# Kernel tuning notes

Measured on AMD Instinct MI355X. Metric: run time of the kernel, lower is better.

The kernel has to match this reference:

```python
import jax, jax.numpy as jnp
import numpy as np

N_U = 50000; N_I = 50000; F = 128; H = 128; E = 800000; G = 512; C = 16; L = 3
EPS = 1e-5


def setup_inputs() -> dict:
    key = jax.random.key(0)
    ks = jax.random.split(key, 22)
    s = 1.0 / np.sqrt(H)
    inp = {}
    inp["x_user"] = jax.random.normal(ks[0], (N_U, F), jnp.float32)
    inp["x_item"] = jax.random.normal(ks[1], (N_I, F), jnp.float32)
    inp["edge_u2i"] = jnp.stack([jax.random.randint(ks[2], (E,), 0, N_U),
                                 jax.random.randint(ks[3], (E,), 0, N_I)])
    inp["edge_i2u"] = jnp.stack([jax.random.randint(ks[4], (E,), 0, N_I),
                                 jax.random.randint(ks[5], (E,), 0, N_U)])
    inp["batch_user"] = jnp.sort(jax.random.randint(ks[6], (N_U,), 0, G))
    inp["batch_item"] = jnp.sort(jax.random.randint(ks[7], (N_I,), 0, G))
    # GraphConv params per layer per relation (in-dim == hidden == 128, so stackable)
    inp["Wrel_u2i"] = jax.random.uniform(ks[8], (L, H, F), jnp.float32, -s, s)
    inp["Wroot_u2i"] = jax.random.uniform(ks[9], (L, H, F), jnp.float32, -s, s)
    inp["b_u2i"] = jax.random.uniform(ks[10], (L, H), jnp.float32, -s, s)
    inp["Wrel_i2u"] = jax.random.uniform(ks[11], (L, H, F), jnp.float32, -s, s)
    inp["Wroot_i2u"] = jax.random.uniform(ks[12], (L, H, F), jnp.float32, -s, s)
    inp["b_i2u"] = jax.random.uniform(ks[13], (L, H), jnp.float32, -s, s)
    # BatchNorm (one module per node type, reused across layers)
    inp["bn_g_user"] = jnp.ones((H,), jnp.float32)
    inp["bn_b_user"] = jnp.zeros((H,), jnp.float32)
    inp["bn_g_item"] = jnp.ones((H,), jnp.float32)
    inp["bn_b_item"] = jnp.zeros((H,), jnp.float32)
    # per-layer classifier heads
    inp["fc_W"] = jax.random.uniform(ks[14], (L, C, H), jnp.float32, -s, s)
    inp["fc_b"] = jax.random.uniform(ks[15], (L, C), jnp.float32, -s, s)
    return inp


def _graph_conv(x_src, x_dst, edge, Wrel, Wroot, b, n_dst):
    # GraphConv, aggr='add': W_rel @ sum_{j in N(i)} x_j + W_root @ x_i + b
    agg = jax.ops.segment_sum(x_src[edge[0]], edge[1], num_segments=n_dst)  # [n_dst, F]
    return agg @ Wrel.T + x_dst @ Wroot.T + b


def _bn(x, g, b):
    # BatchNorm1d over nodes, training-mode batch statistics (biased var)
    m = x.mean(0)
    v = jnp.mean((x - m) ** 2, axis=0)
    return (x - m) * jax.lax.rsqrt(v + EPS) * g + b


def reference(x_user, x_item, edge_u2i, edge_i2u, batch_user, batch_item,
              Wrel_u2i, Wroot_u2i, b_u2i, Wrel_i2u, Wroot_i2u, b_i2u,
              bn_g_user, bn_b_user, bn_g_item, bn_b_item, fc_W, fc_b):
    batch_all = jnp.concatenate([batch_user, batch_item])
    cnt = jax.ops.segment_sum(jnp.ones((N_U + N_I,), jnp.float32), batch_all,
                              num_segments=G)
    cnt = jnp.maximum(cnt, 1.0)[:, None]
    feats = []
    xu, xi = x_user, x_item
    for l in range(L):
        new_i = _graph_conv(xu, xi, edge_u2i, Wrel_u2i[l], Wroot_u2i[l], b_u2i[l], N_I)
        new_u = _graph_conv(xi, xu, edge_i2u, Wrel_i2u[l], Wroot_i2u[l], b_i2u[l], N_U)
        xu = _bn(jax.nn.relu(new_u), bn_g_user, bn_b_user)
        xi = _bn(jax.nn.relu(new_i), bn_g_item, bn_b_item)
        pooled = jax.ops.segment_sum(jnp.concatenate([xu, xi], 0), batch_all,
                                     num_segments=G) / cnt  # global mean pool [G, H]
        feats.append(pooled)
    feats = jnp.stack(feats)  # [L, G, H]
    # eval mode: F.dropout is identity; per-layer linear heads
    logits = jnp.einsum('lgh,lch->lgc', feats, fc_W) + fc_b[:, None, :]  # [L, G, C]
    return (logits, feats)
```

## Files before the change

kernel.cpp:

```cpp
#include <hip/hip_runtime.h>

#define NN 50000
#define FD 128
#define NE 800000
#define NG 512
#define NC 16
#define NL 3
#define NTOT 100000
#define NBLK 391
#define NBUCK 196
#define CAP 10240
#define BINTILE 2048
#define NBINBLK 782
#define BNEPS 1e-5f
#define LOGITS_N (NL*NG*NC)

typedef unsigned short u16;
typedef unsigned char u8;
typedef __attribute__((ext_vector_type(8))) short short8;
typedef __attribute__((ext_vector_type(4))) float f32x4;

#define OFF_GCNT     0ul
#define OFF_BCUR     4096ul
#define OFF_ACC      5120ul
#define MEMSET_BYTES 7168ul
#define OFF_USTART   7680ul
#define OFF_ISTART   10240ul
#define OFF_INVCNT   12800ul
#define OFF_BNSC     14848ul
#define OFF_BNSH     15872ul
#define OFF_ROWRANGE 16896ul
#define OFF_WB       817152ul
#define OFF_CSR      1210368ul
#define OFF_N0I      9238528ul
#define OFF_N0U      22038528ul
#define OFF_N1U      34838528ul
#define OFF_N1I      47638528ul
#define OFF_XU0      60438528ul
#define OFF_XI0      73238528ul
#define OFF_WBS      73238528ul
#define OFF_BVEC     73369600ul

static __device__ __forceinline__ float bf2f(u16 v) {
  return __uint_as_float(((unsigned)v) << 16);
}
static __device__ __forceinline__ u16 f2bf(float f) {
  unsigned u = __float_as_uint(f);
  return (u16)((u + 0x7FFFu + ((u >> 16) & 1u)) >> 16);
}
template<int RELU>
static __device__ __forceinline__ void accT8(float* a, int4 v) {
  unsigned w[4] = {(unsigned)v.x, (unsigned)v.y, (unsigned)v.z, (unsigned)v.w};
  #pragma unroll
  for (int i = 0; i < 4; i++) {
    float lo = __uint_as_float(w[i] << 16);
    float hi = __uint_as_float(w[i] & 0xffff0000u);
    if (RELU) { lo = lo > 0.f ? lo : 0.f; hi = hi > 0.f ? hi : 0.f; }
    a[2*i]   += lo;
    a[2*i+1] += hi;
  }
}
static __device__ __forceinline__ void unp8(float* a, int4 v) {
  a[0] = __uint_as_float(((unsigned)v.x) << 16);
  a[1] = __uint_as_float(((unsigned)v.x) & 0xffff0000u);
  a[2] = __uint_as_float(((unsigned)v.y) << 16);
  a[3] = __uint_as_float(((unsigned)v.y) & 0xffff0000u);
  a[4] = __uint_as_float(((unsigned)v.z) << 16);
  a[5] = __uint_as_float(((unsigned)v.z) & 0xffff0000u);
  a[6] = __uint_as_float(((unsigned)v.w) << 16);
  a[7] = __uint_as_float(((unsigned)v.w) & 0xffff0000u);
}
static __device__ __forceinline__ int relu2(int w) {
  int lo = (w & 0x00008000) ? 0 : (w & 0x0000FFFF);
  int hi = (w < 0)          ? 0 : (int)(w & 0xFFFF0000u);
  return lo | hi;
}

__global__ __launch_bounds__(256) void k_hist_batch(const int* __restrict__ bu,
                                                    const int* __restrict__ bi,
                                                    int* __restrict__ gcnt) {
  int i = blockIdx.x*256 + threadIdx.x;
  if (i >= NTOT) return;
  int type = i >= NN;
  int g = type ? bi[i-NN] : bu[i];
  atomicAdd(&gcnt[type*NG + g], 1);
}

__global__ __launch_bounds__(512) void k_scan_g(const int* __restrict__ gcnt,
                                                int* __restrict__ ustart,
                                                int* __restrict__ istart,
                                                float* __restrict__ invcnt) {
  __shared__ int pu[512], pi[512];
  int t = threadIdx.x;
  int cu = gcnt[t], ci = gcnt[NG + t];
  pu[t] = cu; pi[t] = ci;
  __syncthreads();
  for (int off = 1; off < 512; off <<= 1) {
    int vu = (t >= off) ? pu[t-off] : 0;
    int vi = (t >= off) ? pi[t-off] : 0;
    __syncthreads();
    pu[t] += vu; pi[t] += vi;
    __syncthreads();
  }
  ustart[t] = pu[t] - cu;
  istart[t] = pi[t] - ci;
  if (t == 511) { ustart[NG] = pu[511]; istart[NG] = pi[511]; }
  int c = cu + ci;
  invcnt[t] = 1.0f / (float)(c > 0 ? c : 1);
}

__global__ __launch_bounds__(256) void k_bin(const int* __restrict__ eu2i,
                                             const int* __restrict__ ei2u,
                                             int* __restrict__ bcursor,
                                             int* __restrict__ binned) {
  __shared__ int hist[256];
  __shared__ int scan[256];
  __shared__ int gbase[256];
  __shared__ int rbuf[BINTILE];
  __shared__ u8 rbk[BINTILE];
  int tid = threadIdx.x;
  int base = blockIdx.x * BINTILE;
  hist[tid] = 0;
  __syncthreads();
  int packr[8], bkr[8], rankr[8];
  #pragma unroll
  for (int c = 0; c < 8; c++) {
    int idx = base + c*256 + tid;
    if (idx < 2*NE) {
      int rel = idx >= NE;
      int e = rel ? idx - NE : idx;
      const int* edge = rel ? ei2u : eu2i;
      int s = edge[e];
      int d = edge[NE + e];
      int slot = d + (rel ? NN : 0);
      int bk = slot >> 9;
      bkr[c] = bk;
      packr[c] = ((slot & 511) << 17) | s;
      rankr[c] = atomicAdd(&hist[bk], 1);
    } else bkr[c] = -1;
  }
  __syncthreads();
  scan[tid] = hist[tid];
  __syncthreads();
  for (int o = 1; o < 256; o <<= 1) {
    int v = (tid >= o) ? scan[tid - o] : 0;
    __syncthreads();
    scan[tid] += v;
    __syncthreads();
  }
  if (tid < NBUCK && hist[tid] > 0)
    gbase[tid] = atomicAdd(&bcursor[tid], hist[tid]);
  __syncthreads();
  #pragma unroll
  for (int c = 0; c < 8; c++) {
    if (bkr[c] >= 0) {
      int bk = bkr[c];
      int lpos = scan[bk] - hist[bk] + rankr[c];
      rbuf[lpos] = packr[c];
      rbk[lpos] = (u8)bk;
    }
  }
  __syncthreads();
  int nv = min(BINTILE, 2*NE - base);
  for (int j = tid; j < nv; j += 256) {
    int bk = rbk[j];
    int outpos = bk*CAP + gbase[bk] + (j - (scan[bk] - hist[bk]));
    binned[outpos] = rbuf[j];
  }
}

__global__ __launch_bounds__(256) void k_csrbuild(const int* __restrict__ bcursor,
                                                  int* __restrict__ csrbin,
                                                  int2* __restrict__ rowrange) {
  __shared__ int lcnt[512];
  __shared__ int scan2[256];
  __shared__ int lcsr[CAP];
  int b = blockIdx.x;
  int tid = threadIdx.x;
  int slot0 = b << 9;
  int nslots = min(512, NTOT - slot0);
  int n = bcursor[b];
  int gb = b * CAP;
  lcnt[tid] = 0; lcnt[tid + 256] = 0;
  __syncthreads();
  for (int i = tid; i < n; i += 256) {
    int e = csrbin[gb + i];
    atomicAdd(&lcnt[e >> 17], 1);
  }
  __syncthreads();
  int v0 = lcnt[2*tid], v1 = lcnt[2*tid + 1];
  int ps = v0 + v1;
  scan2[tid] = ps;
  __syncthreads();
  for (int o = 1; o < 256; o <<= 1) {
    int v = (tid >= o) ? scan2[tid - o] : 0;
    __syncthreads();
    scan2[tid] += v;
    __syncthreads();
  }
  int e0 = scan2[tid] - ps;
  int e1 = e0 + v0;
  if (2*tid < nslots)     rowrange[slot0 + 2*tid]     = make_int2(gb + e0, gb + e0 + v0);
  if (2*tid + 1 < nslots) rowrange[slot0 + 2*tid + 1] = make_int2(gb + e1, gb + e1 + v1);
  __syncthreads();
  lcnt[2*tid] = e0; lcnt[2*tid + 1] = e1;
  __syncthreads();
  for (int i = tid; i < n; i += 256) {
    int e = csrbin[gb + i];
    int pos = atomicAdd(&lcnt[e >> 17], 1);
    lcsr[pos] = e & 0x1FFFF;
  }
  __syncthreads();
  for (int i = tid; i < n; i += 256) csrbin[gb + i] = lcsr[i];
}

__global__ __launch_bounds__(256) void k_castX(const float* __restrict__ xu,
                                               const float* __restrict__ xi,
                                               u16* __restrict__ xbu,
                                               u16* __restrict__ xbi) {
  int b = blockIdx.x;
  int half = b >= 6250;
  const float* src = half ? xi : xu;
  u16* dst = half ? xbi : xbu;
  int i = ((half ? b - 6250 : b)*256 + threadIdx.x) * 4;
  float4 v = *(const float4*)(src + i);
  ushort4 o = { f2bf(v.x), f2bf(v.y), f2bf(v.z), f2bf(v.w) };
  *(ushort4*)(dst + i) = o;
}

__global__ __launch_bounds__(256) void k_castW(const float* __restrict__ WrelA,
                                               const float* __restrict__ WrootA,
                                               const float* __restrict__ WrelB,
                                               const float* __restrict__ WrootB,
                                               u16* __restrict__ WB) {
  int idx = blockIdx.x*256 + threadIdx.x;
  int lr = idx >> 15;
  int rem = idx & 32767;
  int h = rem >> 8;
  int k = rem & 255;
  int l = lr >> 1;
  int rel = lr & 1;
  const float* Wr = rel ? WrelB : WrelA;
  const float* Wo = rel ? WrootB : WrootA;
  float v = (k < FD) ? Wr[(l*FD + h)*FD + k] : Wo[(l*FD + h)*FD + (k-FD)];
  WB[idx] = f2bf(v);
}

__global__ __launch_bounds__(256) void k_bnfold(const float* __restrict__ WrelA,
                                                const float* __restrict__ WrootA,
                                                const float* __restrict__ WrelB,
                                                const float* __restrict__ WrootB,
                                                int l,
                                                const float* __restrict__ bnsc,
                                                const float* __restrict__ bnsh,
                                                u16* __restrict__ WBs,
                                                float* __restrict__ bvec) {
  int b = blockIdx.x, tid = threadIdx.x;
  if (b < 64) {
    int e = b*256 + tid;
    int rel = e >> 13;
    int rem = e & 8191;
    int h = rem >> 6;
    int k0 = (rem & 63) * 4;
    const float* Wr = rel ? WrelB : WrelA;
    const float* Wo = rel ? WrootB : WrootA;
    const float* scs = bnsc + (rel ? 128 : 0);
    const float* scd = bnsc + (rel ? 0 : 128);
    u16 t[4];
    #pragma unroll
    for (int j = 0; j < 4; j++) {
      int k = k0 + j;
      float v = (k < FD) ? Wr[((size_t)l*FD + h)*FD + k] * scs[k]
                         : Wo[((size_t)l*FD + h)*FD + (k - FD)] * scd[k - FD];
      t[j] = f2bf(v);
    }
    ushort4 o = { t[0], t[1], t[2], t[3] };
    *(ushort4*)(WBs + rel*32768 + h*256 + k0) = o;
  } else {
    int vid = (b - 64)*256 + tid;
    int kind = vid >> 8;
    int rel = (vid >> 7) & 1;
    int h = vid & 127;
    const float* W = kind ? (rel ? WrootB : WrootA) : (rel ? WrelB : WrelA);
    const float* sh = bnsh + ((kind ^ rel) ? 128 : 0);
    const float* wrow = W + ((size_t)l*FD + h)*FD;
    float s = 0.f;
    #pragma unroll
    for (int k = 0; k < FD; k += 4) {
      float4 wv = *(const float4*)(wrow + k);
      float4 sv = *(const float4*)(sh + k);
      s += wv.x*sv.x + wv.y*sv.y + wv.z*sv.z + wv.w*sv.w;
    }
    bvec[kind*256 + rel*128 + h] = s;
  }
}

template<int RELU>
__global__ __launch_bounds__(256) void k_gather(const u16* __restrict__ curU,
                                                const u16* __restrict__ curI,
                                                const int2* __restrict__ rowrange,
                                                const int* __restrict__ csr,
                                                u16* __restrict__ aggI,
                                                u16* __restrict__ aggU) {
  int b = blockIdx.x;
  int half = b >= 12500;
  int blk = half ? b - 12500 : b;
  const u16* src = half ? curI : curU;
  u16* out = half ? aggU : aggI;
  int slotbase = half ? NN : 0;
  int wid = __builtin_amdgcn_readfirstlane(threadIdx.x >> 6);
  int row = blk*4 + wid;
  int lane = threadIdx.x & 63;
  int q = lane >> 4;
  int c16 = (lane & 15) * 8;
  const u16* sp = src + c16;
  int2 pr = rowrange[slotbase + row];
  int p = pr.x, pe = pr.y;
  float a0[8], a1[8];
  #pragma unroll
  for (int j = 0; j < 8; j++) { a0[j] = 0.f; a1[j] = 0.f; }
  if (p + 8 <= pe) {
    int i0 = csr[p + q], i1 = csr[p + 4 + q];
    while (p + 16 <= pe) {
      int n0 = csr[p + 8 + q], n1 = csr[p + 12 + q];
      int4 v0 = *(const int4*)(sp + (size_t)i0*FD);
      int4 v1 = *(const int4*)(sp + (size_t)i1*FD);
      accT8<RELU>(a0, v0); accT8<RELU>(a1, v1);
      i0 = n0; i1 = n1; p += 8;
    }
    int4 v0 = *(const int4*)(sp + (size_t)i0*FD);
    int4 v1 = *(const int4*)(sp + (size_t)i1*FD);
    accT8<RELU>(a0, v0); accT8<RELU>(a1, v1);
    p += 8;
  }
  int rem = pe - p;
  if (q < rem) {
    int s = csr[p + q];
    accT8<RELU>(a0, *(const int4*)(sp + (size_t)s*FD));
  }
  if (q + 4 < rem) {
    int s = csr[p + 4 + q];
    accT8<RELU>(a1, *(const int4*)(sp + (size_t)s*FD));
  }
  #pragma unroll
  for (int j = 0; j < 8; j++) a0[j] += a1[j];
  #pragma unroll
  for (int j = 0; j < 8; j++) {
    a0[j] += __shfl_xor(a0[j], 16);
    a0[j] += __shfl_xor(a0[j], 32);
  }
  if (q == 0) {
    int4 o;
    o.x = (unsigned)f2bf(a0[0]) | ((unsigned)f2bf(a0[1]) << 16);
    o.y = (unsigned)f2bf(a0[2]) | ((unsigned)f2bf(a0[3]) << 16);
    o.z = (unsigned)f2bf(a0[4]) | ((unsigned)f2bf(a0[5]) << 16);
    o.w = (unsigned)f2bf(a0[6]) | ((unsigned)f2bf(a0[7]) << 16);
    *(int4*)(out + (size_t)row*FD + c16) = o;
  }
}

__global__ __launch_bounds__(256) void k_gemm(u16* __restrict__ newU,
                                              u16* __restrict__ newI,
                                              const u16* __restrict__ curU,
                                              const u16* __restrict__ curI,
                                              const u16* __restrict__ WBl,
                                              const float* __restrict__ bI2U,
                                              const float* __restrict__ bU2I,
                                              float* __restrict__ accSQ,
                                              const float* __restrict__ bvec,
                                              const int2* __restrict__ rowrange,
                                              int fold) {
  __shared__ u16 As[128*72];
  __shared__ u16 Bs[128*72];
  __shared__ float Sred[2][4][128];
  int ty = blockIdx.y;
  u16* A1 = ty ? newI : newU;
  const u16* A2 = ty ? curI : curU;
  const u16* WBp = ty ? WBl : (WBl + 32768);
  const float* bias = ty ? bU2I : bI2U;
  const float* b1p = bvec + (ty ? 0 : 128);
  const float* b2p = bvec + 256 + (ty ? 0 : 128);
  int slot0 = ty ? 0 : NN;
  int tid = threadIdx.x;
  int n0 = blockIdx.x * 128;
  int w = __builtin_amdgcn_readfirstlane(tid >> 6);
  int lane = tid & 63;
  int l15 = lane & 15;
  int quad = lane >> 4;
  f32x4 acc[2][8];
  #pragma unroll
  for (int tr = 0; tr < 2; tr++)
    #pragma unroll
    for (int tc = 0; tc < 8; tc++)
      acc[tr][tc] = (f32x4){0.f,0.f,0.f,0.f};

  for (int ch = 0; ch < 4; ch++) {
    const u16* Ap = (ch < 2) ? ((const u16*)A1 + ch*64) : (A2 + (ch-2)*64);
    int dorelu = fold && (ch >= 2);
    #pragma unroll
    for (int i = 0; i < 4; i++) {
      int e = i*256 + tid;
      int r = e >> 3, seg = e & 7;
      int4 v = {0,0,0,0};
      int gr = n0 + r;
      if (gr < NN) v = *(const int4*)(Ap + (size_t)gr*FD + seg*8);
      if (dorelu) { v.x = relu2(v.x); v.y = relu2(v.y); v.z = relu2(v.z); v.w = relu2(v.w); }
      *(int4*)&As[r*72 + seg*8] = v;
    }
    #pragma unroll
    for (int i = 0; i < 4; i++) {
      int e = i*256 + tid;
      int r = e >> 3, seg = e & 7;
      int4 v = *(const int4*)(WBp + r*256 + ch*64 + seg*8);
      *(int4*)&Bs[r*72 + seg*8] = v;
    }
    __syncthreads();
    #pragma unroll
    for (int ks = 0; ks < 2; ks++) {
      int kb = ks*32 + quad*8;
      short8 af0 = *(const short8*)&As[(w*32 + l15)*72 + kb];
      short8 af1 = *(const short8*)&As[(w*32 + 16 + l15)*72 + kb];
      short8 bf[8];
      #pragma unroll
      for (int tc = 0; tc < 8; tc++)
        bf[tc] = *(const short8*)&Bs[(tc*16 + l15)*72 + kb];
      #pragma unroll
      for (int tc = 0; tc < 8; tc++) {
        acc[0][tc] = __builtin_amdgcn_mfma_f32_16x16x32_bf16(af0, bf[tc], acc[0][tc], 0, 0, 0);
        acc[1][tc] = __builtin_amdgcn_mfma_f32_16x16x32_bf16(af1, bf[tc], acc[1][tc], 0, 0, 0);
      }
    }
    __syncthreads();
  }
  float sv[8], qv[8], bj[8], b1j[8];
  #pragma unroll
  for (int tc = 0; tc < 8; tc++) {
    int col = tc*16 + l15;
    float base = bias[col];
    if (fold) { base += b2p[col]; b1j[tc] = b1p[col]; } else b1j[tc] = 0.f;
    bj[tc] = base;
    sv[tc] = 0.f; qv[tc] = 0.f;
  }
  float dg[2][4] = {{0.f,0.f,0.f,0.f},{0.f,0.f,0.f,0.f}};
  if (fold) {
    #pragma unroll
    for (int tr = 0; tr < 2; tr++)
      #pragma unroll
      for (int gq = 0; gq < 4; gq++) {
        int r = n0 + w*32 + tr*16 + quad*4 + gq;
        if (r < NN) {
          int2 rr = rowrange[slot0 + r];
          dg[tr][gq] = (float)(rr.y - rr.x);
        }
      }
  }
  #pragma unroll
  for (int tr = 0; tr < 2; tr++) {
    int rbase = n0 + w*32 + tr*16 + quad*4;
    #pragma unroll
    for (int tc = 0; tc < 8; tc++) {
      int col = tc*16 + l15;
      #pragma unroll
      for (int g = 0; g < 4; g++) {
        int r = rbase + g;
        if (r < NN) {
          float v = acc[tr][tc][g] + bj[tc] + dg[tr][g]*b1j[tc];
          float y = v > 0.f ? v : 0.f;
          sv[tc] += y; qv[tc] += y*y;
          A1[(size_t)r*FD + col] = f2bf(v);
        }
      }
    }
  }
  #pragma unroll
  for (int tc = 0; tc < 8; tc++) {
    sv[tc] += __shfl_xor(sv[tc], 16); qv[tc] += __shfl_xor(qv[tc], 16);
    sv[tc] += __shfl_xor(sv[tc], 32); qv[tc] += __shfl_xor(qv[tc], 32);
  }
  if (quad == 0) {
    #pragma unroll
    for (int tc = 0; tc < 8; tc++) {
      Sred[0][w][tc*16 + l15] = sv[tc];
      Sred[1][w][tc*16 + l15] = qv[tc];
    }
  }
  __syncthreads();
  if (tid < 128) {
    float s = Sred[0][0][tid] + Sred[0][1][tid] + Sred[0][2][tid] + Sred[0][3][tid];
    float q = Sred[1][0][tid] + Sred[1][1][tid] + Sred[1][2][tid] + Sred[1][3][tid];
    atomicAdd(&accSQ[ty*128 + tid], s);
    atomicAdd(&accSQ[256 + ty*128 + tid], q);
  }
}

__global__ __launch_bounds__(256) void k_bnfinal(float* __restrict__ accSQ,
                                                 const float* __restrict__ gu,
                                                 const float* __restrict__ bu,
                                                 const float* __restrict__ gi,
                                                 const float* __restrict__ bi,
                                                 float* __restrict__ bnsc,
                                                 float* __restrict__ bnsh) {
  int tid = threadIdx.x;
  int type = tid >> 7;
  int c = tid & 127;
  float s = accSQ[tid];
  float q = accSQ[256 + tid];
  accSQ[tid] = 0.f;
  accSQ[256 + tid] = 0.f;
  float inv = 1.0f / (float)NN;
  float mean = s * inv;
  float var = q * inv - mean*mean;
  float rstd = rsqrtf(var + BNEPS);
  float g = type ? gi[c] : gu[c];
  float bb = type ? bi[c] : bu[c];
  float sc = rstd * g;
  bnsc[tid] = sc;
  bnsh[tid] = bb - mean * sc;
}

__global__ __launch_bounds__(256) void k_pool(const u16* __restrict__ newU,
                                              const u16* __restrict__ newI,
                                              const int* __restrict__ ustart,
                                              const int* __restrict__ istart,
                                              const float* __restrict__ bnsc,
                                              const float* __restrict__ bnsh,
                                              const float* __restrict__ invcnt,
                                              float* __restrict__ feats) {
  __shared__ float red[16][128];
  int tid = threadIdx.x;
  int g = blockIdx.x;
  int rt = tid >> 4;
  int c8 = (tid & 15) * 8;
  float tot[8];
  #pragma unroll
  for (int j = 0; j < 8; j++) tot[j] = 0.f;
  #pragma unroll
  for (int type = 0; type < 2; type++) {
    const u16* in = type ? newI : newU;
    const int* st = type ? istart : ustart;
    int rs = st[g], re = st[g+1];
    float acc[8];
    #pragma unroll
    for (int j = 0; j < 8; j++) acc[j] = 0.f;
    int r = rs + rt;
    for (; r + 16 < re; r += 32) {
      int4 v0 = *(const int4*)(in + (size_t)r*FD + c8);
      int4 v1 = *(const int4*)(in + (size_t)(r+16)*FD + c8);
      float f0[8], f1[8];
      unp8(f0, v0); unp8(f1, v1);
      #pragma unroll
      for (int j = 0; j < 8; j++)
        acc[j] += (f0[j] > 0.f ? f0[j] : 0.f) + (f1[j] > 0.f ? f1[j] : 0.f);
    }
    for (; r < re; r += 16) {
      int4 v0 = *(const int4*)(in + (size_t)r*FD + c8);
      float f0[8];
      unp8(f0, v0);
      #pragma unroll
      for (int j = 0; j < 8; j++) acc[j] += f0[j] > 0.f ? f0[j] : 0.f;
    }
    #pragma unroll
    for (int j = 0; j < 8; j++) tot[j] += acc[j] * bnsc[type*128 + c8 + j];
    if (rt == 0) {
      float cnt = (float)(re - rs);
      #pragma unroll
      for (int j = 0; j < 8; j++) tot[j] += cnt * bnsh[type*128 + c8 + j];
    }
  }
  #pragma unroll
  for (int j = 0; j < 8; j++) red[rt][c8 + j] = tot[j];
  __syncthreads();
  if (tid < 128) {
    float s = 0.f;
    #pragma unroll
    for (int i = 0; i < 16; i++) s += red[i][tid];
    feats[(size_t)g*FD + tid] = s * invcnt[g];
  }
}

__global__ __launch_bounds__(256) void k_heads(const float* __restrict__ feats,
                                               const float* __restrict__ fcW,
                                               const float* __restrict__ fcb,
                                               float* __restrict__ logits) {
  int idx = blockIdx.x*256 + threadIdx.x;
  if (idx >= LOGITS_N) return;
  int l = idx >> 13;
  int rem = idx & 8191;
  int g = rem >> 4;
  int c = rem & 15;
  const float* f = feats + ((size_t)l*NG + g)*FD;
  const float* w = fcW + ((size_t)l*NC + c)*FD;
  float s = 0.f;
  #pragma unroll
  for (int k = 0; k < FD; k += 4) {
    float4 fv = *(const float4*)(f + k);
    float4 wv = *(const float4*)(w + k);
    s += fv.x*wv.x + fv.y*wv.y + fv.z*wv.z + fv.w*wv.w;
  }
  logits[idx] = s + fcb[l*NC + c];
}

extern "C" void kernel_launch(void* const* d_in, const int* in_sizes, int n_in,
                              void* d_out, int out_size, void* d_ws, size_t ws_size,
                              hipStream_t stream) {
  const float* x_user   = (const float*)d_in[0];
  const float* x_item   = (const float*)d_in[1];
  const int*   eu2i     = (const int*)d_in[2];
  const int*   ei2u     = (const int*)d_in[3];
  const int*   bu       = (const int*)d_in[4];
  const int*   bi       = (const int*)d_in[5];
  const float* Wrel_u2i = (const float*)d_in[6];
  const float* Wroot_u2i= (const float*)d_in[7];
  const float* b_u2i    = (const float*)d_in[8];
  const float* Wrel_i2u = (const float*)d_in[9];
  const float* Wroot_i2u= (const float*)d_in[10];
  const float* b_i2u    = (const float*)d_in[11];
  const float* bn_g_user= (const float*)d_in[12];
  const float* bn_b_user= (const float*)d_in[13];
  const float* bn_g_item= (const float*)d_in[14];
  const float* bn_b_item= (const float*)d_in[15];
  const float* fcW      = (const float*)d_in[16];
  const float* fcb      = (const float*)d_in[17];

  char* ws = (char*)d_ws;
  int*   gcnt   = (int*)(ws + OFF_GCNT);
  int*   bcursor= (int*)(ws + OFF_BCUR);
  float* accSQ  = (float*)(ws + OFF_ACC);
  int*   ustart = (int*)(ws + OFF_USTART);
  int*   istart = (int*)(ws + OFF_ISTART);
  float* invcnt = (float*)(ws + OFF_INVCNT);
  float* bnsc   = (float*)(ws + OFF_BNSC);
  float* bnsh   = (float*)(ws + OFF_BNSH);
  int2*  rowrange = (int2*)(ws + OFF_ROWRANGE);
  u16*   WB     = (u16*)(ws + OFF_WB);
  int*   csrbin = (int*)(ws + OFF_CSR);
  u16*   n0I    = (u16*)(ws + OFF_N0I);
  u16*   n0U    = (u16*)(ws + OFF_N0U);
  u16*   n1U    = (u16*)(ws + OFF_N1U);
  u16*   n1I    = (u16*)(ws + OFF_N1I);
  u16*   xu0    = (u16*)(ws + OFF_XU0);
  u16*   xi0    = (u16*)(ws + OFF_XI0);
  u16*   WBs    = (u16*)(ws + OFF_WBS);
  float* bvec   = (float*)(ws + OFF_BVEC);
  float* fout   = (float*)d_out;
  float* featsAll = fout + LOGITS_N;

  hipMemsetAsync(ws, 0, MEMSET_BYTES, stream);
  k_hist_batch<<<NBLK, 256, 0, stream>>>(bu, bi, gcnt);
  k_bin<<<NBINBLK, 256, 0, stream>>>(eu2i, ei2u, bcursor, csrbin);
  k_scan_g<<<1, 512, 0, stream>>>(gcnt, ustart, istart, invcnt);
  k_csrbuild<<<NBUCK, 256, 0, stream>>>(bcursor, csrbin, rowrange);
  k_castX<<<12500, 256, 0, stream>>>(x_user, x_item, xu0, xi0);
  k_castW<<<256, 256, 0, stream>>>(Wrel_u2i, Wroot_u2i, Wrel_i2u, Wroot_i2u, WB);

  k_gather<0><<<25000, 256, 0, stream>>>(xu0, xi0, rowrange, csrbin, n0I, n0U);
  k_gemm<<<dim3(NBLK,2), 256, 0, stream>>>(n0U, n0I, xu0, xi0, WB,
                                           b_i2u, b_u2i, accSQ,
                                           bvec, rowrange, 0);
  k_bnfinal<<<1, 256, 0, stream>>>(accSQ, bn_g_user, bn_b_user,
                                   bn_g_item, bn_b_item, bnsc, bnsh);
  k_bnfold<<<66, 256, 0, stream>>>(Wrel_u2i, Wroot_u2i, Wrel_i2u, Wroot_i2u,
                                   1, bnsc, bnsh, WBs, bvec);
  k_pool<<<NG, 256, 0, stream>>>(n0U, n0I, ustart, istart, bnsc, bnsh,
                                 invcnt, featsAll);

  k_gather<1><<<25000, 256, 0, stream>>>(n0U, n0I, rowrange, csrbin, n1I, n1U);
  k_gemm<<<dim3(NBLK,2), 256, 0, stream>>>(n1U, n1I, n0U, n0I, WBs,
                                           b_i2u + FD, b_u2i + FD, accSQ,
                                           bvec, rowrange, 1);
  k_bnfinal<<<1, 256, 0, stream>>>(accSQ, bn_g_user, bn_b_user,
                                   bn_g_item, bn_b_item, bnsc, bnsh);
  k_bnfold<<<66, 256, 0, stream>>>(Wrel_u2i, Wroot_u2i, Wrel_i2u, Wroot_i2u,
                                   2, bnsc, bnsh, WBs, bvec);
  k_pool<<<NG, 256, 0, stream>>>(n1U, n1I, ustart, istart, bnsc, bnsh,
                                 invcnt, featsAll + NG*FD);

  k_gather<1><<<25000, 256, 0, stream>>>(n1U, n1I, rowrange, csrbin, n0I, n0U);
  k_gemm<<<dim3(NBLK,2), 256, 0, stream>>>(n0U, n0I, n1U, n1I, WBs,
                                           b_i2u + 2*FD, b_u2i + 2*FD, accSQ,
                                           bvec, rowrange, 1);
  k_bnfinal<<<1, 256, 0, stream>>>(accSQ, bn_g_user, bn_b_user,
                                   bn_g_item, bn_b_item, bnsc, bnsh);
  k_pool<<<NG, 256, 0, stream>>>(n0U, n0I, ustart, istart, bnsc, bnsh,
                                 invcnt, featsAll + 2*NG*FD);

  k_heads<<<96, 256, 0, stream>>>(featsAll, fcW, fcb, fout);
}
```

Baseline: 535.9 us.

## Fuse BN finalize into weight fold and stage GEMM output through LDS

The BN statistics finalization is merged into the weight-folding kernel: every block recomputes scale and shift into shared memory, the last block writes them out, and the accSQ reset moves into the pool kernel. This removes three tiny single-block launches. The GEMM epilogue now writes bf16 results into shared memory, reusing the A/B tile buffer, and then stores full rows with 16-byte vector writes instead of scattered 2-byte stores. The cost is an extra LDS round trip and a barrier in the epilogue, plus redundant BN math in each fold block.

Result: faster. 521.9 us (-2.6%).

```diff
diff --git a/kernel.cpp b/kernel.cpp
--- a/kernel.cpp
+++ b/kernel.cpp
@@ -246,17 +246,44 @@
   WB[idx] = f2bf(v);
 }
 
-__global__ __launch_bounds__(256) void k_bnfold(const float* __restrict__ WrelA,
-                                                const float* __restrict__ WrootA,
-                                                const float* __restrict__ WrelB,
-                                                const float* __restrict__ WrootB,
-                                                int l,
-                                                const float* __restrict__ bnsc,
-                                                const float* __restrict__ bnsh,
-                                                u16* __restrict__ WBs,
-                                                float* __restrict__ bvec) {
-  int b = blockIdx.x, tid = threadIdx.x;
-  if (b < 64) {
+__global__ __launch_bounds__(256) void k_bnfold2(const float* __restrict__ WrelA,
+                                                 const float* __restrict__ WrootA,
+                                                 const float* __restrict__ WrelB,
+                                                 const float* __restrict__ WrootB,
+                                                 int l,
+                                                 const float* __restrict__ accSQ,
+                                                 const float* __restrict__ gu,
+                                                 const float* __restrict__ bu_,
+                                                 const float* __restrict__ gi,
+                                                 const float* __restrict__ bi_,
+                                                 u16* __restrict__ WBs,
+                                                 float* __restrict__ bvec,
+                                                 float* __restrict__ bnsc,
+                                                 float* __restrict__ bnsh) {
+  __shared__ float sc_l[256], sh_l[256];
+  int tid = threadIdx.x;
+  {
+    int type = tid >> 7;
+    int c = tid & 127;
+    float s = accSQ[tid];
+    float q = accSQ[256 + tid];
+    float inv = 1.0f / (float)NN;
+    float mean = s * inv;
+    float var = q * inv - mean*mean;
+    float rstd = rsqrtf(var + BNEPS);
+    float g = type ? gi[c] : gu[c];
+    float bb = type ? bi_[c] : bu_[c];
+    float sc = rstd * g;
+    sc_l[tid] = sc;
+    sh_l[tid] = bb - mean * sc;
+  }
+  __syncthreads();
+  int b = blockIdx.x;
+  int lastb = gridDim.x - 1;
+  if (b == lastb) {
+    bnsc[tid] = sc_l[tid];
+    bnsh[tid] = sh_l[tid];
+  } else if (b < 64) {
     int e = b*256 + tid;
     int rel = e >> 13;
     int rem = e & 8191;
@@ -264,8 +291,8 @@
     int k0 = (rem & 63) * 4;
     const float* Wr = rel ? WrelB : WrelA;
     const float* Wo = rel ? WrootB : WrootA;
-    const float* scs = bnsc + (rel ? 128 : 0);
-    const float* scd = bnsc + (rel ? 0 : 128);
+    const float* scs = sc_l + (rel ? 128 : 0);
+    const float* scd = sc_l + (rel ? 0 : 128);
     u16 t[4];
     #pragma unroll
     for (int j = 0; j < 4; j++) {
@@ -282,13 +309,13 @@
     int rel = (vid >> 7) & 1;
     int h = vid & 127;
     const float* W = kind ? (rel ? WrootB : WrootA) : (rel ? WrelB : WrelA);
-    const float* sh = bnsh + ((kind ^ rel) ? 128 : 0);
+    const float* sh = sh_l + ((kind ^ rel) ? 128 : 0);
     const float* wrow = W + ((size_t)l*FD + h)*FD;
     float s = 0.f;
     #pragma unroll
     for (int k = 0; k < FD; k += 4) {
       float4 wv = *(const float4*)(wrow + k);
-      float4 sv = *(const float4*)(sh + k);
+      float4 sv = { sh[k], sh[k+1], sh[k+2], sh[k+3] };
       s += wv.x*sv.x + wv.y*sv.y + wv.z*sv.z + wv.w*sv.w;
     }
     bvec[kind*256 + rel*128 + h] = s;
@@ -370,9 +397,11 @@
                                               const float* __restrict__ bvec,
                                               const int2* __restrict__ rowrange,
                                               int fold) {
-  __shared__ u16 As[128*72];
-  __shared__ u16 Bs[128*72];
+  __shared__ u16 smem[128*72*2];
   __shared__ float Sred[2][4][128];
+  u16* As = smem;
+  u16* Bs = smem + 128*72;
+  u16* Cs = smem;
   int ty = blockIdx.y;
   u16* A1 = ty ? newI : newU;
   const u16* A2 = ty ? curI : curU;
@@ -456,18 +485,19 @@
   }
   #pragma unroll
   for (int tr = 0; tr < 2; tr++) {
-    int rbase = n0 + w*32 + tr*16 + quad*4;
+    int rl0 = w*32 + tr*16 + quad*4;
+    int rbase = n0 + rl0;
     #pragma unroll
     for (int tc = 0; tc < 8; tc++) {
       int col = tc*16 + l15;
       #pragma unroll
       for (int g = 0; g < 4; g++) {
         int r = rbase + g;
+        float v = acc[tr][tc][g] + bj[tc] + dg[tr][g]*b1j[tc];
+        Cs[(rl0 + g)*132 + col] = f2bf(v);
         if (r < NN) {
-          float v = acc[tr][tc][g] + bj[tc] + dg[tr][g]*b1j[tc];
           float y = v > 0.f ? v : 0.f;
           sv[tc] += y; qv[tc] += y*y;
-          A1[(size_t)r*FD + col] = f2bf(v);
         }
       }
     }
@@ -491,31 +521,15 @@
     atomicAdd(&accSQ[ty*128 + tid], s);
     atomicAdd(&accSQ[256 + ty*128 + tid], q);
   }
-}
-
-__global__ __launch_bounds__(256) void k_bnfinal(float* __restrict__ accSQ,
-                                                 const float* __restrict__ gu,
-                                                 const float* __restrict__ bu,
-                                                 const float* __restrict__ gi,
-                                                 const float* __restrict__ bi,
-                                                 float* __restrict__ bnsc,
-                                                 float* __restrict__ bnsh) {
-  int tid = threadIdx.x;
-  int type = tid >> 7;
-  int c = tid & 127;
-  float s = accSQ[tid];
-  float q = accSQ[256 + tid];
-  accSQ[tid] = 0.f;
-  accSQ[256 + tid] = 0.f;
-  float inv = 1.0f / (float)NN;
-  float mean = s * inv;
-  float var = q * inv - mean*mean;
-  float rstd = rsqrtf(var + BNEPS);
-  float g = type ? gi[c] : gu[c];
-  float bb = type ? bi[c] : bu[c];
-  float sc = rstd * g;
-  bnsc[tid] = sc;
-  bnsh[tid] = bb - mean * sc;
+  int prow = tid >> 4;
+  int pc = (tid & 15) * 8;
+  #pragma unroll
+  for (int j = 0; j < 8; j++) {
+    int row = j*16 + prow;
+    int gr = n0 + row;
+    int4 vv = *(const int4*)&Cs[row*132 + pc];
+    if (gr < NN) *(int4*)(A1 + (size_t)gr*FD + pc) = vv;
+  }
 }
 
 __global__ __launch_bounds__(256) void k_pool(const u16* __restrict__ newU,
@@ -525,10 +539,12 @@
                                               const float* __restrict__ bnsc,
                                               const float* __restrict__ bnsh,
                                               const float* __restrict__ invcnt,
-                                              float* __restrict__ feats) {
+                                              float* __restrict__ feats,
+                                              float* __restrict__ accSQ) {
   __shared__ float red[16][128];
   int tid = threadIdx.x;
   int g = blockIdx.x;
+  if (g == 0) { accSQ[tid] = 0.f; accSQ[256 + tid] = 0.f; }
   int rt = tid >> 4;
   int c8 = (tid & 15) * 8;
   float tot[8];
@@ -657,32 +673,31 @@
   k_gemm<<<dim3(NBLK,2), 256, 0, stream>>>(n0U, n0I, xu0, xi0, WB,
                                            b_i2u, b_u2i, accSQ,
                                            bvec, rowrange, 0);
-  k_bnfinal<<<1, 256, 0, stream>>>(accSQ, bn_g_user, bn_b_user,
-                                   bn_g_item, bn_b_item, bnsc, bnsh);
-  k_bnfold<<<66, 256, 0, stream>>>(Wrel_u2i, Wroot_u2i, Wrel_i2u, Wroot_i2u,
-                                   1, bnsc, bnsh, WBs, bvec);
+  k_bnfold2<<<67, 256, 0, stream>>>(Wrel_u2i, Wroot_u2i, Wrel_i2u, Wroot_i2u,
+                                    1, accSQ, bn_g_user, bn_b_user,
+                                    bn_g_item, bn_b_item, WBs, bvec, bnsc, bnsh);
   k_pool<<<NG, 256, 0, stream>>>(n0U, n0I, ustart, istart, bnsc, bnsh,
-                                 invcnt, featsAll);
+                                 invcnt, featsAll, accSQ);
 
   k_gather<1><<<25000, 256, 0, stream>>>(n0U, n0I, rowrange, csrbin, n1I, n1U);
   k_gemm<<<dim3(NBLK,2), 256, 0, stream>>>(n1U, n1I, n0U, n0I, WBs,
                                            b_i2u + FD, b_u2i + FD, accSQ,
                                            bvec, rowrange, 1);
-  k_bnfinal<<<1, 256, 0, stream>>>(accSQ, bn_g_user, bn_b_user,
-                                   bn_g_item, bn_b_item, bnsc, bnsh);
-  k_bnfold<<<66, 256, 0, stream>>>(Wrel_u2i, Wroot_u2i, Wrel_i2u, Wroot_i2u,
-                                   2, bnsc, bnsh, WBs, bvec);
+  k_bnfold2<<<67, 256, 0, stream>>>(Wrel_u2i, Wroot_u2i, Wrel_i2u, Wroot_i2u,
+                                    2, accSQ, bn_g_user, bn_b_user,
+                                    bn_g_item, bn_b_item, WBs, bvec, bnsc, bnsh);
   k_pool<<<NG, 256, 0, stream>>>(n1U, n1I, ustart, istart, bnsc, bnsh,
-                                 invcnt, featsAll + NG*FD);
+                                 invcnt, featsAll + NG*FD, accSQ);
 
   k_gather<1><<<25000, 256, 0, stream>>>(n1U, n1I, rowrange, csrbin, n0I, n0U);
   k_gemm<<<dim3(NBLK,2), 256, 0, stream>>>(n0U, n0I, n1U, n1I, WBs,
                                            b_i2u + 2*FD, b_u2i + 2*FD, accSQ,
                                            bvec, rowrange, 1);
-  k_bnfinal<<<1, 256, 0, stream>>>(accSQ, bn_g_user, bn_b_user,
-                                   bn_g_item, bn_b_item, bnsc, bnsh);
+  k_bnfold2<<<1, 256, 0, stream>>>(Wrel_u2i, Wroot_u2i, Wrel_i2u, Wroot_i2u,
+                                   2, accSQ, bn_g_user, bn_b_user,
+                                   bn_g_item, bn_b_item, WBs, bvec, bnsc, bnsh);
   k_pool<<<NG, 256, 0, stream>>>(n0U, n0I, ustart, istart, bnsc, bnsh,
-                                 invcnt, featsAll + 2*NG*FD);
+                                 invcnt, featsAll + 2*NG*FD, accSQ);
 
   k_heads<<<96, 256, 0, stream>>>(featsAll, fcW, fcb, fout);
 }
```
